# Optimization experiments

Hardware: AMD Instinct MI355X
Metric: run time of the kernel (lower is better)

## Reference

```python
import jax, jax.numpy as jnp
import numpy as np

HID, BOT, C, HEADS, K, SCALES, HZN = 32, 8, 16, 4, 3, 4, 12


def layer_norm(x, g, b, eps=1e-5):
    m = jnp.mean(x, axis=-1, keepdims=True)
    v = jnp.var(x, axis=-1, keepdims=True)
    return (x - m) * jax.lax.rsqrt(v + eps) * g + b


def setup_inputs() -> dict:
    B, T, N = 8, 32, 1500
    keys = iter(jax.random.split(jax.random.key(0), 64))
    def nrm(shape, s=0.05):
        return jax.random.normal(next(keys), shape, jnp.float32) * s
    x = jax.random.normal(next(keys), (B, T, N), jnp.float32)
    adj = (jax.random.uniform(next(keys), (N, N)) < 0.01).astype(jnp.float32)
    return dict(
        x=x, adj=adj,
        dw_w=nrm((1, 1, K)), dw_b=jnp.zeros((1,)),
        bn1_g=jnp.ones((1,)), bn1_b=jnp.zeros((1,)),
        pw_w=nrm((C, 1)), pw_b=jnp.zeros((C,)),
        bn2_g=jnp.ones((C,)), bn2_b=jnp.zeros((C,)),
        feat_w=nrm((C, HID)), feat_b=jnp.zeros((HID,)),
        scale_w=nrm((SCALES, HID, HID)), scale_b=jnp.zeros((SCALES, HID)),
        scale_ln_g=jnp.ones((SCALES, HID)), scale_ln_b=jnp.zeros((SCALES, HID)),
        fusion_weight=jnp.exp(-0.5 * jnp.arange(SCALES, dtype=jnp.float32)),
        fus_lo_w=nrm((HID, BOT)), fus_lo_b=jnp.zeros((BOT,)),
        fus_hi_w=nrm((BOT, HID)), fus_hi_b=jnp.zeros((HID,)),
        sp_ln_g=jnp.ones((HID,)), sp_ln_b=jnp.zeros((HID,)),
        qkv_lo_w=nrm((HID, 3 * BOT)), qkv_lo_b=jnp.zeros((3 * BOT,)),
        qkv_hi_w=nrm((3 * BOT, 3 * HID)), qkv_hi_b=jnp.zeros((3 * HID,)),
        graph_U=nrm((N, BOT)), graph_V=nrm((BOT, N)),
        adj_mix=jnp.array(0.0, jnp.float32), adj_scale=jnp.array(1.0, jnp.float32),
        out_lo_w=nrm((HID, BOT)), out_lo_b=jnp.zeros((BOT,)),
        out_hi_w=nrm((BOT, HID)), out_hi_b=jnp.zeros((HID,)),
        at_ln_g=jnp.ones((HID,)), at_ln_b=jnp.zeros((HID,)),
        pred_lo_w=nrm((HID, BOT)), pred_lo_b=jnp.zeros((BOT,)),
        mid_ln_g=jnp.ones((BOT,)), mid_ln_b=jnp.zeros((BOT,)),
        pred_hi_w=nrm((BOT, HZN)), pred_hi_b=jnp.zeros((HZN,)),
        log_decay=jnp.array(-2.3, jnp.float32),
        gate_w1=nrm((HID, BOT)), gate_b1=jnp.zeros((BOT,)),
        gate_w2=nrm((BOT, HZN)), gate_b2=jnp.zeros((HZN,)),
    )


def reference(x, adj, dw_w, dw_b, bn1_g, bn1_b, pw_w, pw_b, bn2_g, bn2_b,
              feat_w, feat_b, scale_w, scale_b, scale_ln_g, scale_ln_b,
              fusion_weight, fus_lo_w, fus_lo_b, fus_hi_w, fus_hi_b,
              sp_ln_g, sp_ln_b, qkv_lo_w, qkv_lo_b, qkv_hi_w, qkv_hi_b,
              graph_U, graph_V, adj_mix, adj_scale,
              out_lo_w, out_lo_b, out_hi_w, out_hi_b, at_ln_g, at_ln_b,
              pred_lo_w, pred_lo_b, mid_ln_g, mid_ln_b, pred_hi_w, pred_hi_b,
              log_decay, gate_w1, gate_b1, gate_w2, gate_b2):
    B, T, N = x.shape
    # ---- temporal feature extraction: depthwise-separable conv, eval-mode BN ----
    s = x.transpose(0, 2, 1).reshape(B * N, 1, T)  # per-node series [B*N,1,T]
    dw = jax.lax.conv_general_dilated(
        s, dw_w, (1,), 'SAME', dimension_numbers=('NCH', 'OIH', 'NCH'))
    dw = jax.nn.relu((dw + dw_b[None, :, None]) * bn1_g[None, :, None] + bn1_b[None, :, None])
    pw = jnp.einsum('bit,oi->bot', dw, pw_w) + pw_b[None, :, None]  # pointwise 1x1
    pw = jax.nn.relu(pw * bn2_g[None, :, None] + bn2_b[None, :, None])
    h = pw.mean(-1).reshape(B, N, C) @ feat_w + feat_b  # [B,N,HID]
    # ---- multi-scale spatial diffusion over adjacency powers ----
    eye = jnp.eye(N, dtype=x.dtype)
    a_hat = adj + eye
    a_hat = a_hat / (jnp.sum(a_hat, axis=-1, keepdims=True) + 1e-8)
    a2 = a_hat @ a_hat
    hops = [eye, a_hat, a2, a2 @ a_hat]
    feats = []
    for i in range(SCALES):  # fixed, small loop over scales
        agg = h if i == 0 else jnp.einsum('nm,bmh->bnh', hops[i], h)
        t = agg @ scale_w[i] + scale_b[i]
        feats.append(jax.nn.relu(layer_norm(t, scale_ln_g[i], scale_ln_b[i])))
    alpha = jax.nn.softmax(fusion_weight)
    fused = sum(alpha[i] * feats[i] for i in range(SCALES))
    out = (fused @ fus_lo_w + fus_lo_b) @ fus_hi_w + fus_hi_b  # bottleneck fusion
    h = layer_norm(out + h, sp_ln_g, sp_ln_b)
    # ---- low-rank adaptive graph attention ----
    qkv = (h @ qkv_lo_w + qkv_lo_b) @ qkv_hi_w + qkv_hi_b  # [B,N,3*HID]
    q, k, v = jnp.split(qkv, 3, axis=-1)
    hd = HID // HEADS
    to_heads = lambda t: t.reshape(B, N, HEADS, hd).transpose(0, 2, 1, 3)
    q, k, v = to_heads(q), to_heads(k), to_heads(v)
    scores = jnp.einsum('bhnd,bhmd->bhnm', q, k) / jnp.sqrt(jnp.float32(hd))
    struct = graph_U @ graph_V + jax.nn.sigmoid(adj_mix) * adj_scale * adj  # [N,N]
    attn = jax.nn.softmax(scores + struct[None, None], axis=-1)
    o = jnp.einsum('bhnm,bhmd->bhnd', attn, v).transpose(0, 2, 1, 3).reshape(B, N, HID)
    o = (o @ out_lo_w + out_lo_b) @ out_hi_w + out_hi_b
    h = layer_norm(o + h, at_ln_g, at_ln_b)
    # ---- gated horizon predictor with learned exponential decay ----
    x_mid = jax.nn.relu(layer_norm(h @ pred_lo_w + pred_lo_b, mid_ln_g, mid_ln_b))
    init_pred = x_mid @ pred_hi_w + pred_hi_b  # [B,N,HZN]
    gate = jax.nn.sigmoid(jax.nn.relu(h @ gate_w1 + gate_b1) @ gate_w2 + gate_b2)
    tdec = jnp.arange(1, HZN + 1, dtype=x.dtype)  # [HZN]
    prog = x[:, -1, :, None] * jnp.exp(-jnp.exp(log_decay) * tdec)
    return gate * init_pred + (1.0 - gate) * prog
```

## Files before the change

### kernel.cpp

```cpp
#include <hip/hip_runtime.h>
#include <math.h>

#define NN 1500
#define BB 8
#define TT 32
#define HIDD 32
#define BOTT 8
#define CC 16
#define NHEADS 4
#define NSCALES 4
#define HZNN 12
#define BC (BB*HIDD)
#define CAP 128
#define MC 128
#define MSPLIT 2
#define RT 64
#define NTILES 24
#define PROWS (NTILES*RT)

__global__ void k_prep_temporal(const float* __restrict__ adj,
                                const float* __restrict__ gV,
                                int* __restrict__ sidx, float* __restrict__ sval,
                                float* __restrict__ sraw, int* __restrict__ scnt,
                                float* __restrict__ VgT,
                                const float* __restrict__ x,
    const float* __restrict__ dw_w, const float* __restrict__ dw_b,
    const float* __restrict__ bn1_g, const float* __restrict__ bn1_b,
    const float* __restrict__ pw_w, const float* __restrict__ pw_b,
    const float* __restrict__ bn2_g, const float* __restrict__ bn2_b,
    const float* __restrict__ feat_w, const float* __restrict__ feat_b,
    float* __restrict__ h0) {
  if (blockIdx.x < NN) {
    int n = blockIdx.x;
    int tid = threadIdx.x;
    const float* row = adj + (size_t)n * NN;
    __shared__ int cnt;
    __shared__ float red[4];
    __shared__ float s_inv;
    float ssum = 0.f;
    for (int m = tid; m < NN; m += 256) ssum += row[m];
    for (int off = 32; off > 0; off >>= 1) ssum += __shfl_down(ssum, off, 64);
    if ((tid & 63) == 0) red[tid >> 6] = ssum;
    if (tid == 0) cnt = 0;
    __syncthreads();
    if (tid == 0) {
      float tot = red[0] + red[1] + red[2] + red[3] + 1.0f;
      s_inv = 1.0f / (tot + 1e-8f);
    }
    __syncthreads();
    float inv = s_inv;
    for (int m = tid; m < NN; m += 256) {
      float a = row[m];
      if (a != 0.f || m == n) {
        int pos = atomicAdd(&cnt, 1);
        if (pos < CAP) {
          sidx[n * CAP + pos] = m;
          sval[n * CAP + pos] = (a + (m == n ? 1.f : 0.f)) * inv;
          sraw[n * CAP + pos] = a;
        }
      }
    }
    __syncthreads();
    if (tid == 0) scnt[n] = min(cnt, CAP);
    if (n == 0) {
      for (int m = tid; m < NN; m += 256) {
#pragma unroll
        for (int j = 0; j < 8; ++j) VgT[m * 8 + j] = gV[j * NN + m];
      }
    }
  } else {
    int tid = (blockIdx.x - NN) * 256 + threadIdx.x;
    if (tid >= BB * NN) return;
    int b = tid / NN, n = tid % NN;
    float s[TT];
#pragma unroll
    for (int t = 0; t < TT; ++t) s[t] = x[(size_t)b * TT * NN + (size_t)t * NN + n];
    float w0 = dw_w[0], w1 = dw_w[1], w2 = dw_w[2];
    float db = dw_b[0], g1v = bn1_g[0], b1v = bn1_b[0];
    float dwr[TT];
#pragma unroll
    for (int t = 0; t < TT; ++t) {
      float left  = (t > 0)      ? s[t - 1] : 0.f;
      float right = (t < TT - 1) ? s[t + 1] : 0.f;
      float v = left * w0 + s[t] * w1 + right * w2;
      v = (v + db) * g1v + b1v;
      dwr[t] = fmaxf(v, 0.f);
    }
    float mo[CC];
#pragma unroll
    for (int o = 0; o < CC; ++o) mo[o] = 0.f;
    for (int t = 0; t < TT; ++t) {
      float d = dwr[t];
#pragma unroll
      for (int o = 0; o < CC; ++o) {
        float v = (d * pw_w[o] + pw_b[o]) * bn2_g[o] + bn2_b[o];
        mo[o] += fmaxf(v, 0.f);
      }
    }
#pragma unroll
    for (int o = 0; o < CC; ++o) mo[o] *= (1.f / TT);
    float* dst = h0 + (size_t)n * BC + b * HIDD;
    for (int j = 0; j < HIDD; ++j) {
      float acc = feat_b[j];
#pragma unroll
      for (int o = 0; o < CC; ++o) acc += mo[o] * feat_w[o * HIDD + j];
      dst[j] = acc;
    }
  }
}

__global__ void k_spmm_sp(const int* __restrict__ sidx, const float* __restrict__ sval,
                          const int* __restrict__ scnt,
                          const float* __restrict__ X, float* __restrict__ Y) {
  int n = blockIdx.x;
  int tid = threadIdx.x;
  __shared__ int   li[CAP];
  __shared__ float lv[CAP];
  int cnt = scnt[n];
  if (tid < cnt) { li[tid] = sidx[n * CAP + tid]; lv[tid] = sval[n * CAP + tid]; }
  __syncthreads();
  float acc = 0.f;
  for (int e = 0; e < cnt; ++e) acc += lv[e] * X[(size_t)li[e] * BC + tid];
  Y[(size_t)n * BC + tid] = acc;
}

__global__ void k_fuse_qkv(
    const float* __restrict__ h0, const float* __restrict__ g1,
    const float* __restrict__ g2, const float* __restrict__ g3,
    const float* __restrict__ scale_w, const float* __restrict__ scale_b,
    const float* __restrict__ sln_g, const float* __restrict__ sln_b,
    const float* __restrict__ fusion_w,
    const float* __restrict__ fus_lo_w, const float* __restrict__ fus_lo_b,
    const float* __restrict__ fus_hi_w, const float* __restrict__ fus_hi_b,
    const float* __restrict__ sp_g, const float* __restrict__ sp_b,
    const float* __restrict__ qkv_lo_w, const float* __restrict__ qkv_lo_b,
    const float* __restrict__ qkv_hi_w, const float* __restrict__ qkv_hi_b,
    float* __restrict__ h_out,
    float* __restrict__ Qw, float* __restrict__ Kw, float* __restrict__ Vw) {
  int tid = threadIdx.x;
  int gr = tid >> 3, l = tid & 7;
  int row = blockIdx.x * 32 + gr;
  int b = row / NN, n = row % NN;
  size_t rofs = (size_t)n * BC + b * HIDD;
  int j0 = 4 * l;
  float fw0 = fusion_w[0], fw1 = fusion_w[1], fw2 = fusion_w[2], fw3 = fusion_w[3];
  float fm = fmaxf(fmaxf(fw0, fw1), fmaxf(fw2, fw3));
  float e0 = __expf(fw0 - fm), e1 = __expf(fw1 - fm), e2 = __expf(fw2 - fm), e3 = __expf(fw3 - fm);
  float einv = 1.f / (e0 + e1 + e2 + e3);
  float alpha[4] = {e0 * einv, e1 * einv, e2 * einv, e3 * einv};
  const float* srcp[4] = {h0, g1, g2, g3};
  float fused[4] = {0.f, 0.f, 0.f, 0.f};
#pragma unroll
  for (int i = 0; i < NSCALES; ++i) {
    const float* sp = srcp[i] + rofs;
    float src[32];
#pragma unroll
    for (int k4 = 0; k4 < 8; ++k4) {
      float4 f = *(const float4*)(sp + k4 * 4);
      src[k4 * 4] = f.x; src[k4 * 4 + 1] = f.y; src[k4 * 4 + 2] = f.z; src[k4 * 4 + 3] = f.w;
    }
    const float* W = scale_w + i * HIDD * HIDD;
    float t[4];
#pragma unroll
    for (int jj = 0; jj < 4; ++jj) t[jj] = scale_b[i * HIDD + j0 + jj];
#pragma unroll
    for (int k = 0; k < 32; ++k) {
      float4 w = *(const float4*)(W + k * HIDD + j0);
      t[0] += src[k] * w.x; t[1] += src[k] * w.y; t[2] += src[k] * w.z; t[3] += src[k] * w.w;
    }
    float s1 = t[0] + t[1] + t[2] + t[3];
    float s2 = t[0]*t[0] + t[1]*t[1] + t[2]*t[2] + t[3]*t[3];
    s1 += __shfl_xor(s1, 1, 8); s1 += __shfl_xor(s1, 2, 8); s1 += __shfl_xor(s1, 4, 8);
    s2 += __shfl_xor(s2, 1, 8); s2 += __shfl_xor(s2, 2, 8); s2 += __shfl_xor(s2, 4, 8);
    float mean = s1 * (1.f / 32.f);
    float var = s2 * (1.f / 32.f) - mean * mean;
    float r = rsqrtf(var + 1e-5f);
    float a = alpha[i];
#pragma unroll
    for (int jj = 0; jj < 4; ++jj) {
      float tn = (t[jj] - mean) * r * sln_g[i * HIDD + j0 + jj] + sln_b[i * HIDD + j0 + jj];
      fused[jj] += a * fmaxf(tn, 0.f);
    }
  }
  float lo[BOTT];
#pragma unroll
  for (int o = 0; o < BOTT; ++o) {
    float acc = 0.f;
#pragma unroll
    for (int jj = 0; jj < 4; ++jj) acc += fused[jj] * fus_lo_w[(j0 + jj) * BOTT + o];
    acc += __shfl_xor(acc, 1, 8); acc += __shfl_xor(acc, 2, 8); acc += __shfl_xor(acc, 4, 8);
    lo[o] = acc + fus_lo_b[o];
  }
  float4 hv4 = *(const float4*)(h0 + rofs + j0);
  float hv[4] = {hv4.x, hv4.y, hv4.z, hv4.w};
  float pre[4];
#pragma unroll
  for (int jj = 0; jj < 4; ++jj) {
    float acc = fus_hi_b[j0 + jj] + hv[jj];
#pragma unroll
    for (int o = 0; o < BOTT; ++o) acc += lo[o] * fus_hi_w[o * HIDD + j0 + jj];
    pre[jj] = acc;
  }
  {
    float s1 = pre[0] + pre[1] + pre[2] + pre[3];
    float s2 = pre[0]*pre[0] + pre[1]*pre[1] + pre[2]*pre[2] + pre[3]*pre[3];
    s1 += __shfl_xor(s1, 1, 8); s1 += __shfl_xor(s1, 2, 8); s1 += __shfl_xor(s1, 4, 8);
    s2 += __shfl_xor(s2, 1, 8); s2 += __shfl_xor(s2, 2, 8); s2 += __shfl_xor(s2, 4, 8);
    float mean = s1 * (1.f / 32.f);
    float var = s2 * (1.f / 32.f) - mean * mean;
    float r = rsqrtf(var + 1e-5f);
#pragma unroll
    for (int jj = 0; jj < 4; ++jj)
      pre[jj] = (pre[jj] - mean) * r * sp_g[j0 + jj] + sp_b[j0 + jj];
  }
  *(float4*)(h_out + (size_t)row * HIDD + j0) = make_float4(pre[0], pre[1], pre[2], pre[3]);
  float t1[24];
#pragma unroll
  for (int o = 0; o < 24; ++o) {
    float acc = 0.f;
#pragma unroll
    for (int jj = 0; jj < 4; ++jj) acc += pre[jj] * qkv_lo_w[(j0 + jj) * 24 + o];
    acc += __shfl_xor(acc, 1, 8); acc += __shfl_xor(acc, 2, 8); acc += __shfl_xor(acc, 4, 8);
    t1[o] = acc + qkv_lo_b[o];
  }
#pragma unroll
  for (int part = 0; part < 3; ++part) {
    float* dst = (part == 0) ? Qw : (part == 1) ? Kw : Vw;
#pragma unroll
    for (int hd = 0; hd < NHEADS; ++hd) {
      int p = part * 32 + hd * 8 + l;
      float acc = qkv_hi_b[p];
#pragma unroll
      for (int o = 0; o < 24; ++o) acc += t1[o] * qkv_hi_w[o * 96 + p];
      dst[(((size_t)b * NHEADS + hd) * NN + n) * 8 + l] = acc;
    }
  }
}

__global__ void k_attn(const float* __restrict__ Qw, const float* __restrict__ Kw,
                       const float* __restrict__ Vw,
                       const float* __restrict__ gU, const float* __restrict__ VgT,
                       const int* __restrict__ sidx, const float* __restrict__ sraw,
                       const int* __restrict__ scnt,
                       const float* __restrict__ adj_mix, const float* __restrict__ adj_scale,
                       float* __restrict__ P) {
  int bh = blockIdx.x, tile = blockIdx.y, z = blockIdx.z;
  int tid = threadIdx.x;
  int g = tid >> 3, p = tid & 7;
  __shared__ float Ks[MC * 20];
  __shared__ float Vs[MC * 12];
  const float scl = 0.35355339059327373f;
  float qv[2][16], acc[2][8], sm[2];
  int nrow[2];
#pragma unroll
  for (int rr = 0; rr < 2; ++rr) {
    int n = tile * RT + g * 2 + rr;
    nrow[rr] = n;
    int nc = (n < NN) ? n : NN - 1;
    const float* qp = Qw + ((size_t)bh * NN + nc) * 8;
    float4 q0 = *(const float4*)qp;
    float4 q1 = *(const float4*)(qp + 4);
    const float* up = gU + nc * 8;
    float4 u0 = *(const float4*)up;
    float4 u1 = *(const float4*)(up + 4);
    qv[rr][0] = q0.x * scl; qv[rr][1] = q0.y * scl; qv[rr][2] = q0.z * scl; qv[rr][3] = q0.w * scl;
    qv[rr][4] = q1.x * scl; qv[rr][5] = q1.y * scl; qv[rr][6] = q1.z * scl; qv[rr][7] = q1.w * scl;
    qv[rr][8] = u0.x; qv[rr][9] = u0.y; qv[rr][10] = u0.z; qv[rr][11] = u0.w;
    qv[rr][12] = u1.x; qv[rr][13] = u1.y; qv[rr][14] = u1.z; qv[rr][15] = u1.w;
    sm[rr] = 0.f;
#pragma unroll
    for (int d = 0; d < 8; ++d) acc[rr][d] = 0.f;
  }
  if (z < MSPLIT) {
    const int mcount = NN / MSPLIT;
    const int mbase = z * mcount;
    const float* Kb = Kw + (size_t)bh * NN * 8;
    const float* Vb = Vw + (size_t)bh * NN * 8;
    for (int c0 = 0; c0 < mcount; c0 += MC) {
      int mlen = min(MC, mcount - c0);
      __syncthreads();
      {
        int mm = tid >> 1, hh = tid & 1;
        float4 kf = make_float4(0.f,0.f,0.f,0.f), gf = kf, vf = kf;
        if (mm < mlen) {
          int m = mbase + c0 + mm;
          kf = *(const float4*)(Kb + (size_t)m * 8 + hh * 4);
          gf = *(const float4*)(VgT + (size_t)m * 8 + hh * 4);
          vf = *(const float4*)(Vb + (size_t)m * 8 + hh * 4);
        }
        *(float4*)(Ks + mm * 20 + hh * 4) = kf;
        *(float4*)(Ks + mm * 20 + 8 + hh * 4) = gf;
        *(float4*)(Vs + mm * 12 + hh * 4) = vf;
      }
      __syncthreads();
#pragma unroll 4
      for (int i = 0; i < MC / 8; ++i) {
        int mm = p + i * 8;
        const float* kp = Ks + mm * 20;
        float4 k0 = *(const float4*)(kp);
        float4 k1 = *(const float4*)(kp + 4);
        float4 k2 = *(const float4*)(kp + 8);
        float4 k3 = *(const float4*)(kp + 12);
        const float* vp = Vs + mm * 12;
        float4 v0 = *(const float4*)(vp);
        float4 v1 = *(const float4*)(vp + 4);
#pragma unroll
        for (int rr = 0; rr < 2; ++rr) {
          float s = qv[rr][0]*k0.x + qv[rr][1]*k0.y + qv[rr][2]*k0.z + qv[rr][3]*k0.w
                  + qv[rr][4]*k1.x + qv[rr][5]*k1.y + qv[rr][6]*k1.z + qv[rr][7]*k1.w
                  + qv[rr][8]*k2.x + qv[rr][9]*k2.y + qv[rr][10]*k2.z + qv[rr][11]*k2.w
                  + qv[rr][12]*k3.x + qv[rr][13]*k3.y + qv[rr][14]*k3.z + qv[rr][15]*k3.w;
          float e = __expf(s);
          sm[rr] += e;
          acc[rr][0] += e * v0.x; acc[rr][1] += e * v0.y; acc[rr][2] += e * v0.z; acc[rr][3] += e * v0.w;
          acc[rr][4] += e * v1.x; acc[rr][5] += e * v1.y; acc[rr][6] += e * v1.z; acc[rr][7] += e * v1.w;
        }
      }
      if (mlen < MC) {
        int npad = (MC / 8) - ((mlen - p + 7) >> 3);
        sm[0] -= (float)npad;
        sm[1] -= (float)npad;
      }
    }
  } else {
    float smix = adj_scale[0] / (1.f + __expf(-adj_mix[0]));
    const float* Kb = Kw + (size_t)bh * NN * 8;
    const float* Vb = Vw + (size_t)bh * NN * 8;
#pragma unroll
    for (int rr = 0; rr < 2; ++rr) {
      int n = nrow[rr];
      if (n < NN) {
        int cnt = scnt[n];
        for (int e = p; e < cnt; e += 8) {
          int m = sidx[n * CAP + e];
          float a = sraw[n * CAP + e];
          if (a != 0.f) {
            const float* kp = Kb + (size_t)m * 8;
            float4 k0 = *(const float4*)(kp);
            float4 k1 = *(const float4*)(kp + 4);
            const float* gp = VgT + (size_t)m * 8;
            float4 k2 = *(const float4*)(gp);
            float4 k3 = *(const float4*)(gp + 4);
            float s = qv[rr][0]*k0.x + qv[rr][1]*k0.y + qv[rr][2]*k0.z + qv[rr][3]*k0.w
                    + qv[rr][4]*k1.x + qv[rr][5]*k1.y + qv[rr][6]*k1.z + qv[rr][7]*k1.w
                    + qv[rr][8]*k2.x + qv[rr][9]*k2.y + qv[rr][10]*k2.z + qv[rr][11]*k2.w
                    + qv[rr][12]*k3.x + qv[rr][13]*k3.y + qv[rr][14]*k3.z + qv[rr][15]*k3.w;
            float ep = __expf(s);
            float dlt = ep * (__expf(smix * a) - 1.f);
            sm[rr] += dlt;
            const float* vp = Vb + (size_t)m * 8;
            float4 v0 = *(const float4*)(vp);
            float4 v1 = *(const float4*)(vp + 4);
            acc[rr][0] += dlt * v0.x; acc[rr][1] += dlt * v0.y; acc[rr][2] += dlt * v0.z; acc[rr][3] += dlt * v0.w;
            acc[rr][4] += dlt * v1.x; acc[rr][5] += dlt * v1.y; acc[rr][6] += dlt * v1.z; acc[rr][7] += dlt * v1.w;
          }
        }
      }
    }
  }
#pragma unroll
  for (int rr = 0; rr < 2; ++rr) {
    float s = sm[rr];
    s += __shfl_xor(s, 1, 8); s += __shfl_xor(s, 2, 8); s += __shfl_xor(s, 4, 8);
#pragma unroll
    for (int d = 0; d < 8; ++d) {
      acc[rr][d] += __shfl_xor(acc[rr][d], 1, 8);
      acc[rr][d] += __shfl_xor(acc[rr][d], 2, 8);
      acc[rr][d] += __shfl_xor(acc[rr][d], 4, 8);
    }
    float val = acc[rr][0];
#pragma unroll
    for (int d = 1; d < 8; ++d) if (p == d) val = acc[rr][d];
    if (nrow[rr] < NN) {
      float* dst = P + ((size_t)(z * 32 + bh) * PROWS + nrow[rr]) * 12;
      dst[p] = val;
      if (p == 0) dst[8] = s;
    }
  }
}

__global__ void k_final(const float* __restrict__ P, const float* __restrict__ h_in,
    const float* __restrict__ x,
    const float* __restrict__ out_lo_w, const float* __restrict__ out_lo_b,
    const float* __restrict__ out_hi_w, const float* __restrict__ out_hi_b,
    const float* __restrict__ at_g, const float* __restrict__ at_b,
    const float* __restrict__ pred_lo_w, const float* __restrict__ pred_lo_b,
    const float* __restrict__ mid_g, const float* __restrict__ mid_b,
    const float* __restrict__ pred_hi_w, const float* __restrict__ pred_hi_b,
    const float* __restrict__ log_decay,
    const float* __restrict__ gate_w1, const float* __restrict__ gate_b1,
    const float* __restrict__ gate_w2, const float* __restrict__ gate_b2,
    float* __restrict__ out) {
  int tid = blockIdx.x * 64 + threadIdx.x;
  if (tid >= BB * NN) return;
  int b = tid / NN, n = tid % NN;
  size_t row = (size_t)b * NN + n;
  float ov[HIDD];
#pragma unroll
  for (int hd = 0; hd < NHEADS; ++hd) {
    int bh = b * NHEADS + hd;
    float smt = 0.f, av[8];
#pragma unroll
    for (int d = 0; d < 8; ++d) av[d] = 0.f;
#pragma unroll
    for (int z = 0; z <= MSPLIT; ++z) {
      const float* q = P + ((size_t)(z * 32 + bh) * PROWS + n) * 12;
      smt += q[8];
#pragma unroll
      for (int d = 0; d < 8; ++d) av[d] += q[d];
    }
    float inv = 1.f / smt;
#pragma unroll
    for (int d = 0; d < 8; ++d) ov[hd * 8 + d] = av[d] * inv;
  }
  float lo[BOTT];
  for (int o = 0; o < BOTT; ++o) {
    float acc = out_lo_b[o];
#pragma unroll
    for (int j = 0; j < HIDD; ++j) acc += ov[j] * out_lo_w[j * BOTT + o];
    lo[o] = acc;
  }
  float pre[HIDD];
  for (int j = 0; j < HIDD; ++j) {
    float acc = out_hi_b[j] + h_in[row * HIDD + j];
#pragma unroll
    for (int o = 0; o < BOTT; ++o) acc += lo[o] * out_hi_w[o * HIDD + j];
    pre[j] = acc;
  }
  float m0 = 0.f;
#pragma unroll
  for (int j = 0; j < HIDD; ++j) m0 += pre[j];
  m0 *= (1.f / 32.f);
  float v0 = 0.f;
#pragma unroll
  for (int j = 0; j < HIDD; ++j) { float d = pre[j] - m0; v0 += d * d; }
  v0 *= (1.f / 32.f);
  float r0 = rsqrtf(v0 + 1e-5f);
  float h2[HIDD];
#pragma unroll
  for (int j = 0; j < HIDD; ++j) h2[j] = (pre[j] - m0) * r0 * at_g[j] + at_b[j];
  float pl[BOTT];
  for (int o = 0; o < BOTT; ++o) {
    float acc = pred_lo_b[o];
#pragma unroll
    for (int j = 0; j < HIDD; ++j) acc += h2[j] * pred_lo_w[j * BOTT + o];
    pl[o] = acc;
  }
  float m = 0.f;
#pragma unroll
  for (int o = 0; o < BOTT; ++o) m += pl[o];
  m *= (1.f / BOTT);
  float var = 0.f;
#pragma unroll
  for (int o = 0; o < BOTT; ++o) { float d = pl[o] - m; var += d * d; }
  var *= (1.f / BOTT);
  float rr = rsqrtf(var + 1e-5f);
  float xm[BOTT];
#pragma unroll
  for (int o = 0; o < BOTT; ++o)
    xm[o] = fmaxf((pl[o] - m) * rr * mid_g[o] + mid_b[o], 0.f);
  float initp[HZNN];
  for (int i = 0; i < HZNN; ++i) {
    float acc = pred_hi_b[i];
#pragma unroll
    for (int o = 0; o < BOTT; ++o) acc += xm[o] * pred_hi_w[o * HZNN + i];
    initp[i] = acc;
  }
  float ga[BOTT];
  for (int o = 0; o < BOTT; ++o) {
    float acc = gate_b1[o];
#pragma unroll
    for (int j = 0; j < HIDD; ++j) acc += h2[j] * gate_w1[j * BOTT + o];
    ga[o] = fmaxf(acc, 0.f);
  }
  float xl = x[(size_t)b * TT * NN + (size_t)(TT - 1) * NN + n];
  float dec = expf(log_decay[0]);
  for (int i = 0; i < HZNN; ++i) {
    float acc = gate_b2[i];
#pragma unroll
    for (int o = 0; o < BOTT; ++o) acc += ga[o] * gate_w2[o * HZNN + i];
    float gt = 1.f / (1.f + expf(-acc));
    float pr = xl * expf(-dec * (float)(i + 1));
    out[row * HZNN + i] = gt * initp[i] + (1.f - gt) * pr;
  }
}

extern "C" void kernel_launch(void* const* d_in, const int* in_sizes, int n_in,
                              void* d_out, int out_size, void* d_ws, size_t ws_size,
                              hipStream_t stream) {
  const float* x          = (const float*)d_in[0];
  const float* adj        = (const float*)d_in[1];
  const float* dw_w       = (const float*)d_in[2];
  const float* dw_b       = (const float*)d_in[3];
  const float* bn1_g      = (const float*)d_in[4];
  const float* bn1_b      = (const float*)d_in[5];
  const float* pw_w       = (const float*)d_in[6];
  const float* pw_b       = (const float*)d_in[7];
  const float* bn2_g      = (const float*)d_in[8];
  const float* bn2_b      = (const float*)d_in[9];
  const float* feat_w     = (const float*)d_in[10];
  const float* feat_b     = (const float*)d_in[11];
  const float* scale_w    = (const float*)d_in[12];
  const float* scale_b    = (const float*)d_in[13];
  const float* scale_ln_g = (const float*)d_in[14];
  const float* scale_ln_b = (const float*)d_in[15];
  const float* fusion_w   = (const float*)d_in[16];
  const float* fus_lo_w   = (const float*)d_in[17];
  const float* fus_lo_b   = (const float*)d_in[18];
  const float* fus_hi_w   = (const float*)d_in[19];
  const float* fus_hi_b   = (const float*)d_in[20];
  const float* sp_ln_g    = (const float*)d_in[21];
  const float* sp_ln_b    = (const float*)d_in[22];
  const float* qkv_lo_w   = (const float*)d_in[23];
  const float* qkv_lo_b   = (const float*)d_in[24];
  const float* qkv_hi_w   = (const float*)d_in[25];
  const float* qkv_hi_b   = (const float*)d_in[26];
  const float* graph_U    = (const float*)d_in[27];
  const float* graph_V    = (const float*)d_in[28];
  const float* adj_mix    = (const float*)d_in[29];
  const float* adj_scale  = (const float*)d_in[30];
  const float* out_lo_w   = (const float*)d_in[31];
  const float* out_lo_b   = (const float*)d_in[32];
  const float* out_hi_w   = (const float*)d_in[33];
  const float* out_hi_b   = (const float*)d_in[34];
  const float* at_ln_g    = (const float*)d_in[35];
  const float* at_ln_b    = (const float*)d_in[36];
  const float* pred_lo_w  = (const float*)d_in[37];
  const float* pred_lo_b  = (const float*)d_in[38];
  const float* mid_ln_g   = (const float*)d_in[39];
  const float* mid_ln_b   = (const float*)d_in[40];
  const float* pred_hi_w  = (const float*)d_in[41];
  const float* pred_hi_b  = (const float*)d_in[42];
  const float* log_decay  = (const float*)d_in[43];
  const float* gate_w1    = (const float*)d_in[44];
  const float* gate_b1    = (const float*)d_in[45];
  const float* gate_w2    = (const float*)d_in[46];
  const float* gate_b2    = (const float*)d_in[47];

  float* ws = (float*)d_ws;
  float* h0    = ws;
  float* g1    = h0 + (size_t)NN * BC;
  float* g2    = g1 + (size_t)NN * BC;
  float* g3    = g2 + (size_t)NN * BC;
  float* hfull = g3 + (size_t)NN * BC;
  float* Qw    = hfull + (size_t)BB * NN * HIDD;
  float* Kw    = Qw + (size_t)BB * NN * HIDD;
  float* Vw    = Kw + (size_t)BB * NN * HIDD;
  float* VgT   = Vw + (size_t)BB * NN * HIDD;
  float* sval  = VgT + (size_t)NN * 8;
  float* sraw  = sval + (size_t)NN * CAP;
  int*   sidx  = (int*)(sraw + (size_t)NN * CAP);
  int*   scnt  = sidx + (size_t)NN * CAP;
  float* P     = (float*)(scnt + NN + 3);
  P = (float*)(((uintptr_t)P + 15) & ~(uintptr_t)15);

  k_prep_temporal<<<NN + 47, 256, 0, stream>>>(
      adj, graph_V, sidx, sval, sraw, scnt, VgT,
      x, dw_w, dw_b, bn1_g, bn1_b, pw_w, pw_b, bn2_g, bn2_b, feat_w, feat_b, h0);
  k_spmm_sp<<<NN, 256, 0, stream>>>(sidx, sval, scnt, h0, g1);
  k_spmm_sp<<<NN, 256, 0, stream>>>(sidx, sval, scnt, g1, g2);
  k_spmm_sp<<<NN, 256, 0, stream>>>(sidx, sval, scnt, g2, g3);
  k_fuse_qkv<<<(BB * NN) / 32, 256, 0, stream>>>(
      h0, g1, g2, g3, scale_w, scale_b, scale_ln_g, scale_ln_b, fusion_w,
      fus_lo_w, fus_lo_b, fus_hi_w, fus_hi_b, sp_ln_g, sp_ln_b,
      qkv_lo_w, qkv_lo_b, qkv_hi_w, qkv_hi_b, hfull, Qw, Kw, Vw);
  k_attn<<<dim3(32, NTILES, MSPLIT + 1), 256, 0, stream>>>(
      Qw, Kw, Vw, graph_U, VgT, sidx, sraw, scnt, adj_mix, adj_scale, P);
  k_final<<<(BB * NN + 63) / 64, 64, 0, stream>>>(
      P, hfull, x, out_lo_w, out_lo_b, out_hi_w, out_hi_b, at_ln_g, at_ln_b,
      pred_lo_w, pred_lo_b, mid_ln_g, mid_ln_b, pred_hi_w, pred_hi_b,
      log_decay, gate_w1, gate_b1, gate_w2, gate_b2, (float*)d_out);
}
```

Before: 294.9 us.

## Process four query rows per thread in attention and parallelize final epilogue across lanes

```diff
diff --git a/kernel.cpp b/kernel.cpp
--- a/kernel.cpp
+++ b/kernel.cpp
@@ -14,8 +14,8 @@
 #define CAP 128
 #define MC 128
 #define MSPLIT 2
-#define RT 64
-#define NTILES 24
+#define RT 128
+#define NTILES 12
 #define PROWS (NTILES*RT)
 
 __global__ void k_prep_temporal(const float* __restrict__ adj,
@@ -250,11 +250,11 @@
   __shared__ float Ks[MC * 20];
   __shared__ float Vs[MC * 12];
   const float scl = 0.35355339059327373f;
-  float qv[2][16], acc[2][8], sm[2];
-  int nrow[2];
-#pragma unroll
-  for (int rr = 0; rr < 2; ++rr) {
-    int n = tile * RT + g * 2 + rr;
+  float qv[4][16], acc[4][8], sm[4];
+  int nrow[4];
+#pragma unroll
+  for (int rr = 0; rr < 4; ++rr) {
+    int n = tile * RT + g * 4 + rr;
     nrow[rr] = n;
     int nc = (n < NN) ? n : NN - 1;
     const float* qp = Qw + ((size_t)bh * NN + nc) * 8;
@@ -293,7 +293,7 @@
         *(float4*)(Vs + mm * 12 + hh * 4) = vf;
       }
       __syncthreads();
-#pragma unroll 4
+#pragma unroll 2
       for (int i = 0; i < MC / 8; ++i) {
         int mm = p + i * 8;
         const float* kp = Ks + mm * 20;
@@ -305,7 +305,7 @@
         float4 v0 = *(const float4*)(vp);
         float4 v1 = *(const float4*)(vp + 4);
 #pragma unroll
-        for (int rr = 0; rr < 2; ++rr) {
+        for (int rr = 0; rr < 4; ++rr) {
           float s = qv[rr][0]*k0.x + qv[rr][1]*k0.y + qv[rr][2]*k0.z + qv[rr][3]*k0.w
                   + qv[rr][4]*k1.x + qv[rr][5]*k1.y + qv[rr][6]*k1.z + qv[rr][7]*k1.w
                   + qv[rr][8]*k2.x + qv[rr][9]*k2.y + qv[rr][10]*k2.z + qv[rr][11]*k2.w
@@ -318,8 +318,8 @@
       }
       if (mlen < MC) {
         int npad = (MC / 8) - ((mlen - p + 7) >> 3);
-        sm[0] -= (float)npad;
-        sm[1] -= (float)npad;
+#pragma unroll
+        for (int rr = 0; rr < 4; ++rr) sm[rr] -= (float)npad;
       }
     }
   } else {
@@ -327,7 +327,7 @@
     const float* Kb = Kw + (size_t)bh * NN * 8;
     const float* Vb = Vw + (size_t)bh * NN * 8;
 #pragma unroll
-    for (int rr = 0; rr < 2; ++rr) {
+    for (int rr = 0; rr < 4; ++rr) {
       int n = nrow[rr];
       if (n < NN) {
         int cnt = scnt[n];
@@ -359,7 +359,7 @@
     }
   }
 #pragma unroll
-  for (int rr = 0; rr < 2; ++rr) {
+  for (int rr = 0; rr < 4; ++rr) {
     float s = sm[rr];
     s += __shfl_xor(s, 1, 8); s += __shfl_xor(s, 2, 8); s += __shfl_xor(s, 4, 8);
 #pragma unroll
@@ -391,97 +391,106 @@
     const float* __restrict__ gate_w1, const float* __restrict__ gate_b1,
     const float* __restrict__ gate_w2, const float* __restrict__ gate_b2,
     float* __restrict__ out) {
-  int tid = blockIdx.x * 64 + threadIdx.x;
-  if (tid >= BB * NN) return;
-  int b = tid / NN, n = tid % NN;
-  size_t row = (size_t)b * NN + n;
-  float ov[HIDD];
-#pragma unroll
-  for (int hd = 0; hd < NHEADS; ++hd) {
-    int bh = b * NHEADS + hd;
-    float smt = 0.f, av[8];
-#pragma unroll
-    for (int d = 0; d < 8; ++d) av[d] = 0.f;
-#pragma unroll
-    for (int z = 0; z <= MSPLIT; ++z) {
-      const float* q = P + ((size_t)(z * 32 + bh) * PROWS + n) * 12;
-      smt += q[8];
-#pragma unroll
-      for (int d = 0; d < 8; ++d) av[d] += q[d];
-    }
-    float inv = 1.f / smt;
-#pragma unroll
-    for (int d = 0; d < 8; ++d) ov[hd * 8 + d] = av[d] * inv;
-  }
+  int tid = threadIdx.x;
+  int gr = tid >> 3, l = tid & 7;
+  int row = blockIdx.x * 32 + gr;
+  int b = row / NN, n = row % NN;
+  int j0 = 4 * l;
+  int hd = l >> 1, d0 = (l & 1) * 4;
+  int bh = b * NHEADS + hd;
+  float av[4] = {0.f, 0.f, 0.f, 0.f};
+  float smt = 0.f;
+#pragma unroll
+  for (int z = 0; z <= MSPLIT; ++z) {
+    const float* q = P + ((size_t)(z * 32 + bh) * PROWS + n) * 12;
+    float4 a4 = *(const float4*)(q + d0);
+    av[0] += a4.x; av[1] += a4.y; av[2] += a4.z; av[3] += a4.w;
+    smt += q[8];
+  }
+  float oinv = 1.f / smt;
+  float ov4[4];
+#pragma unroll
+  for (int d = 0; d < 4; ++d) ov4[d] = av[d] * oinv;
   float lo[BOTT];
+#pragma unroll
   for (int o = 0; o < BOTT; ++o) {
-    float acc = out_lo_b[o];
-#pragma unroll
-    for (int j = 0; j < HIDD; ++j) acc += ov[j] * out_lo_w[j * BOTT + o];
-    lo[o] = acc;
-  }
-  float pre[HIDD];
-  for (int j = 0; j < HIDD; ++j) {
-    float acc = out_hi_b[j] + h_in[row * HIDD + j];
-#pragma unroll
-    for (int o = 0; o < BOTT; ++o) acc += lo[o] * out_hi_w[o * HIDD + j];
-    pre[j] = acc;
-  }
-  float m0 = 0.f;
-#pragma unroll
-  for (int j = 0; j < HIDD; ++j) m0 += pre[j];
-  m0 *= (1.f / 32.f);
-  float v0 = 0.f;
-#pragma unroll
-  for (int j = 0; j < HIDD; ++j) { float d = pre[j] - m0; v0 += d * d; }
-  v0 *= (1.f / 32.f);
-  float r0 = rsqrtf(v0 + 1e-5f);
-  float h2[HIDD];
-#pragma unroll
-  for (int j = 0; j < HIDD; ++j) h2[j] = (pre[j] - m0) * r0 * at_g[j] + at_b[j];
+    float acc = 0.f;
+#pragma unroll
+    for (int jj = 0; jj < 4; ++jj) acc += ov4[jj] * out_lo_w[(j0 + jj) * BOTT + o];
+    acc += __shfl_xor(acc, 1, 8); acc += __shfl_xor(acc, 2, 8); acc += __shfl_xor(acc, 4, 8);
+    lo[o] = acc + out_lo_b[o];
+  }
+  float4 hin4 = *(const float4*)(h_in + (size_t)row * HIDD + j0);
+  float pre[4] = {hin4.x, hin4.y, hin4.z, hin4.w};
+#pragma unroll
+  for (int jj = 0; jj < 4; ++jj) {
+    float acc = out_hi_b[j0 + jj] + pre[jj];
+#pragma unroll
+    for (int o = 0; o < BOTT; ++o) acc += lo[o] * out_hi_w[o * HIDD + j0 + jj];
+    pre[jj] = acc;
+  }
+  float h2[4];
+  {
+    float s1 = pre[0] + pre[1] + pre[2] + pre[3];
+    float s2 = pre[0]*pre[0] + pre[1]*pre[1] + pre[2]*pre[2] + pre[3]*pre[3];
+    s1 += __shfl_xor(s1, 1, 8); s1 += __shfl_xor(s1, 2, 8); s1 += __shfl_xor(s1, 4, 8);
+    s2 += __shfl_xor(s2, 1, 8); s2 += __shfl_xor(s2, 2, 8); s2 += __shfl_xor(s2, 4, 8);
+    float mean = s1 * (1.f / 32.f);
+    float var = s2 * (1.f / 32.f) - mean * mean;
+    float r = rsqrtf(var + 1e-5f);
+#pragma unroll
+    for (int jj = 0; jj < 4; ++jj)
+      h2[jj] = (pre[jj] - mean) * r * at_g[j0 + jj] + at_b[j0 + jj];
+  }
   float pl[BOTT];
+#pragma unroll
   for (int o = 0; o < BOTT; ++o) {
-    float acc = pred_lo_b[o];
-#pragma unroll
-    for (int j = 0; j < HIDD; ++j) acc += h2[j] * pred_lo_w[j * BOTT + o];
-    pl[o] = acc;
-  }
-  float m = 0.f;
-#pragma unroll
-  for (int o = 0; o < BOTT; ++o) m += pl[o];
-  m *= (1.f / BOTT);
-  float var = 0.f;
-#pragma unroll
-  for (int o = 0; o < BOTT; ++o) { float d = pl[o] - m; var += d * d; }
-  var *= (1.f / BOTT);
-  float rr = rsqrtf(var + 1e-5f);
+    float acc = 0.f;
+#pragma unroll
+    for (int jj = 0; jj < 4; ++jj) acc += h2[jj] * pred_lo_w[(j0 + jj) * BOTT + o];
+    acc += __shfl_xor(acc, 1, 8); acc += __shfl_xor(acc, 2, 8); acc += __shfl_xor(acc, 4, 8);
+    pl[o] = acc + pred_lo_b[o];
+  }
   float xm[BOTT];
-#pragma unroll
-  for (int o = 0; o < BOTT; ++o)
-    xm[o] = fmaxf((pl[o] - m) * rr * mid_g[o] + mid_b[o], 0.f);
-  float initp[HZNN];
-  for (int i = 0; i < HZNN; ++i) {
-    float acc = pred_hi_b[i];
-#pragma unroll
-    for (int o = 0; o < BOTT; ++o) acc += xm[o] * pred_hi_w[o * HZNN + i];
-    initp[i] = acc;
+  {
+    float m = 0.f;
+#pragma unroll
+    for (int o = 0; o < BOTT; ++o) m += pl[o];
+    m *= (1.f / BOTT);
+    float var = 0.f;
+#pragma unroll
+    for (int o = 0; o < BOTT; ++o) { float d = pl[o] - m; var += d * d; }
+    var *= (1.f / BOTT);
+    float r = rsqrtf(var + 1e-5f);
+#pragma unroll
+    for (int o = 0; o < BOTT; ++o)
+      xm[o] = fmaxf((pl[o] - m) * r * mid_g[o] + mid_b[o], 0.f);
   }
   float ga[BOTT];
+#pragma unroll
   for (int o = 0; o < BOTT; ++o) {
-    float acc = gate_b1[o];
-#pragma unroll
-    for (int j = 0; j < HIDD; ++j) acc += h2[j] * gate_w1[j * BOTT + o];
-    ga[o] = fmaxf(acc, 0.f);
+    float acc = 0.f;
+#pragma unroll
+    for (int jj = 0; jj < 4; ++jj) acc += h2[jj] * gate_w1[(j0 + jj) * BOTT + o];
+    acc += __shfl_xor(acc, 1, 8); acc += __shfl_xor(acc, 2, 8); acc += __shfl_xor(acc, 4, 8);
+    ga[o] = fmaxf(acc + gate_b1[o], 0.f);
   }
   float xl = x[(size_t)b * TT * NN + (size_t)(TT - 1) * NN + n];
-  float dec = expf(log_decay[0]);
-  for (int i = 0; i < HZNN; ++i) {
-    float acc = gate_b2[i];
-#pragma unroll
-    for (int o = 0; o < BOTT; ++o) acc += ga[o] * gate_w2[o * HZNN + i];
-    float gt = 1.f / (1.f + expf(-acc));
-    float pr = xl * expf(-dec * (float)(i + 1));
-    out[row * HZNN + i] = gt * initp[i] + (1.f - gt) * pr;
+  float dec = __expf(log_decay[0]);
+#pragma unroll
+  for (int ii = 0; ii < 2; ++ii) {
+    int i = l + ii * 8;
+    if (i < HZNN) {
+      float accp = pred_hi_b[i];
+#pragma unroll
+      for (int o = 0; o < BOTT; ++o) accp += xm[o] * pred_hi_w[o * HZNN + i];
+      float accg = gate_b2[i];
+#pragma unroll
+      for (int o = 0; o < BOTT; ++o) accg += ga[o] * gate_w2[o * HZNN + i];
+      float gt = 1.f / (1.f + __expf(-accg));
+      float pr = xl * __expf(-dec * (float)(i + 1));
+      out[(size_t)row * HZNN + i] = gt * accp + (1.f - gt) * pr;
+    }
   }
 }
 
@@ -566,7 +575,7 @@
       qkv_lo_w, qkv_lo_b, qkv_hi_w, qkv_hi_b, hfull, Qw, Kw, Vw);
   k_attn<<<dim3(32, NTILES, MSPLIT + 1), 256, 0, stream>>>(
       Qw, Kw, Vw, graph_U, VgT, sidx, sraw, scnt, adj_mix, adj_scale, P);
-  k_final<<<(BB * NN + 63) / 64, 64, 0, stream>>>(
+  k_final<<<(BB * NN) / 32, 256, 0, stream>>>(
       P, hfull, x, out_lo_w, out_lo_b, out_hi_w, out_hi_b, at_ln_g, at_ln_b,
       pred_lo_w, pred_lo_b, mid_ln_g, mid_ln_b, pred_hi_w, pred_hi_b,
       log_decay, gate_w1, gate_b1, gate_w2, gate_b2, (float*)d_out);
```

Result: slower. 551.8 us (+87.2%).
